# Performance work log

Hardware: AMD Instinct MI355X
Metric: run time of the kernel (lower is better)

The kernel has to match this reference:

```python
import jax, jax.numpy as jnp
import numpy as np

N_NODES = 50000
N_EDGES = 1600000
D_FEAT = 64
N_SCALARS = 4
N_GRAPHS = 64
HIDDEN = 128
OUT = 128


def setup_inputs() -> dict:
    key = jax.random.key(0)
    ks = jax.random.split(key, 8)
    x = jax.random.normal(ks[0], (N_NODES, D_FEAT), dtype=jnp.float32)
    scalars = jax.random.normal(ks[1], (N_GRAPHS, N_SCALARS), dtype=jnp.float32)
    batch = jnp.sort(jax.random.randint(ks[2], (N_NODES,), 0, N_GRAPHS))
    edge_index = jax.random.randint(ks[3], (2, N_EDGES), 0, N_NODES)
    d_in = 2 * (D_FEAT + N_SCALARS)  # 136: EdgeConv-style cat([x_i, x_j - x_i])
    W1 = jax.random.normal(ks[4], (d_in, HIDDEN), dtype=jnp.float32) * (1.0 / np.sqrt(d_in))
    b1 = jnp.zeros((HIDDEN,), dtype=jnp.float32)
    W2 = jax.random.normal(ks[5], (HIDDEN, OUT), dtype=jnp.float32) * (1.0 / np.sqrt(HIDDEN))
    b2 = jnp.zeros((OUT,), dtype=jnp.float32)
    return {"x": x, "scalars": scalars, "batch": batch, "edge_index": edge_index,
            "W1": W1, "b1": b1, "W2": W2, "b2": b2}


def reference(x, scalars, batch, edge_index, W1, b1, W2, b2):
    # _reshape_scalars: gather per-graph scalars to nodes via batch index
    s = scalars[batch]                       # [N, n_scalars]
    h = jnp.concatenate([x, s], axis=-1)     # [N, d_feat + n_scalars]
    src, dst = edge_index[0], edge_index[1]  # edge j -> i (PyG convention)
    h_i = h[dst]                             # target node features [E, F]
    h_j = h[src]                             # source node features [E, F]
    m_in = jnp.concatenate([h_i, h_j - h_i], axis=-1)  # [E, 2F]
    m = jax.nn.relu(m_in @ W1 + b1) @ W2 + b2          # edge MLP [E, OUT]
    out = jax.ops.segment_sum(m, dst, num_segments=x.shape[0])  # add-aggregation
    return out
```

## Files before the change

### kernel.cpp

```cpp
#include <hip/hip_runtime.h>

#define N_NODES   50000
#define N_EDGES   1600000
#define D_FEAT    64
#define N_SCALARS 4
#define HIDDEN    128
#define OUT_DIM   128
#define UV_DIM    256

#define SLICE_SH  6
#define SLICE_N   (1 << SLICE_SH)
#define NSLICE    ((N_NODES + SLICE_N - 1) >> SLICE_SH)
#define CAP       2560
#define CAPQ      1024
#define CHUNK     4096

#define N_WAVES   (N_NODES / 16)
#define G1_BLOCKS ((N_WAVES + 3) / 4)
#define BIN_BLOCKS ((N_EDGES + CHUNK - 1) / CHUNK)

typedef __attribute__((ext_vector_type(8))) _Float16 half8;
typedef __attribute__((ext_vector_type(2))) _Float16 half2v;
typedef __attribute__((ext_vector_type(4))) float    f32x4;

__device__ __forceinline__ float wf_elem(const float* W1, int k, int j) {
    float wb = W1[(k + 68) * HIDDEN + (j & 127)];
    return (j < HIDDEN) ? (W1[k * HIDDEN + j] - wb) : wb;
}

__device__ __forceinline__ unsigned char f2bf8(float f) {
    unsigned short h = __builtin_bit_cast(unsigned short, (_Float16)f);
    unsigned r = ((unsigned)h + 0x7Fu + ((h >> 8) & 1u)) >> 8;
    return (unsigned char)r;
}

__device__ __forceinline__ half2v bf8x2_to_h2(unsigned short w) {
    unsigned r = __builtin_amdgcn_perm(0u, (unsigned)w, 0x010C000Cu);
    return __builtin_bit_cast(half2v, r);
}

__global__ __launch_bounds__(256) void prep_kernel(
    const float* __restrict__ W1, const float* __restrict__ b1,
    const float* __restrict__ W2, const float* __restrict__ scalars,
    _Float16* __restrict__ WfT, _Float16* __restrict__ W2T,
    float* __restrict__ SG, int* __restrict__ tails)
{
    const int idx = blockIdx.x * 256 + threadIdx.x;
    {   int j = idx >> 6, k = idx & 63;
        WfT[idx] = (_Float16)wf_elem(W1, k, j); }
    {   int j = idx >> 7, k = idx & 127;
        W2T[idx] = (_Float16)W2[k * OUT_DIM + j]; }
    {   int g = idx >> 8, j = idx & 255;
        float s = (j < HIDDEN) ? b1[j] : 0.f;
        #pragma unroll
        for (int t = 0; t < N_SCALARS; ++t)
            s = fmaf(scalars[g * N_SCALARS + t], wf_elem(W1, D_FEAT + t, j), s);
        SG[idx] = s; }
    if (idx < NSLICE) tails[idx] = 0;
}

__global__ __launch_bounds__(256) void gemm1_bin(
    const float* __restrict__ x, const int* __restrict__ batch,
    const _Float16* __restrict__ WfT, const float* __restrict__ SG,
    _Float16* __restrict__ Uh, unsigned char* __restrict__ Vb8,
    const int* __restrict__ ei, int* __restrict__ tails,
    unsigned* __restrict__ glist)
{
    __shared__ unsigned buf[CHUNK];
    __shared__ int hist[NSLICE];
    __shared__ int binStart[NSLICE];
    __shared__ int cursor[NSLICE];
    __shared__ int gbase[NSLICE];
    __shared__ int scanTmp[256];

    const int tid = threadIdx.x;

    if (blockIdx.x < G1_BLOCKS) {
        const int wid = (blockIdx.x * 256 + tid) >> 6;
        if (wid >= N_WAVES) return;
        const int lane = tid & 63;
        const int quad = lane >> 4;
        const int l15  = lane & 15;
        const int row0 = wid * 16;

        f32x4 acc[16];
        #pragma unroll
        for (int c = 0; c < 16; ++c) { f32x4 z = {0.f,0.f,0.f,0.f}; acc[c] = z; }

        const float* xrow = x + (row0 + l15) * D_FEAT;
        #pragma unroll
        for (int t = 0; t < 2; ++t) {
            const int k0 = 32 * t + quad * 8;
            float4 a0 = *(const float4*)(xrow + k0);
            float4 a1 = *(const float4*)(xrow + k0 + 4);
            half8 af;
            af[0] = (_Float16)a0.x; af[1] = (_Float16)a0.y;
            af[2] = (_Float16)a0.z; af[3] = (_Float16)a0.w;
            af[4] = (_Float16)a1.x; af[5] = (_Float16)a1.y;
            af[6] = (_Float16)a1.z; af[7] = (_Float16)a1.w;
            #pragma unroll
            for (int c = 0; c < 16; ++c) {
                half8 bf = *(const half8*)(WfT + (c * 16 + l15) * 64 + k0);
                acc[c] = __builtin_amdgcn_mfma_f32_16x16x32_f16(af, bf, acc[c], 0, 0, 0);
            }
        }

        int bg[4];
        #pragma unroll
        for (int j = 0; j < 4; ++j) bg[j] = batch[row0 + quad * 4 + j];

        #pragma unroll
        for (int c = 0; c < 16; ++c) {
            const int col = c * 16 + l15;
            #pragma unroll
            for (int j = 0; j < 4; ++j) {
                const int n = row0 + quad * 4 + j;
                float v = acc[c][j] + SG[bg[j] * UV_DIM + col];
                if (col < HIDDEN) Uh[(n << 7) + col] = (_Float16)v;
                else              Vb8[(n << 7) + col - HIDDEN] = f2bf8(v);
            }
        }
        return;
    }

    const int e0  = (blockIdx.x - G1_BLOCKS) * CHUNK;
    const int nE  = min(CHUNK, N_EDGES - e0);

    for (int i = tid; i < NSLICE; i += 256) hist[i] = 0;
    __syncthreads();

    unsigned ent[CHUNK / 256];
    #pragma unroll
    for (int j = 0; j < CHUNK / 256; ++j) {
        int e = e0 + tid + j * 256;
        if (e < N_EDGES) {
            unsigned s = (unsigned)ei[e];
            unsigned d = (unsigned)ei[N_EDGES + e];
            ent[j] = (d << 16) | s;
            atomicAdd(&hist[d >> SLICE_SH], 1);
        } else {
            ent[j] = 0xFFFFFFFFu;
        }
    }
    __syncthreads();

    const int base4 = tid * 4;
    int loc[4];
    int sum = 0;
    #pragma unroll
    for (int k = 0; k < 4; ++k) {
        int b = base4 + k;
        loc[k] = (b < NSLICE) ? hist[b] : 0;
        sum += loc[k];
    }
    scanTmp[tid] = sum;
    __syncthreads();
    for (int d = 1; d < 256; d <<= 1) {
        int v = (tid >= d) ? scanTmp[tid - d] : 0;
        __syncthreads();
        scanTmp[tid] += v;
        __syncthreads();
    }
    int run = (tid == 0) ? 0 : scanTmp[tid - 1];
    #pragma unroll
    for (int k = 0; k < 4; ++k) {
        int b = base4 + k;
        if (b < NSLICE) { binStart[b] = run; cursor[b] = run; run += loc[k]; }
    }
    __syncthreads();

    #pragma unroll
    for (int j = 0; j < CHUNK / 256; ++j) {
        if (ent[j] != 0xFFFFFFFFu) {
            int sl = (int)(ent[j] >> (16 + SLICE_SH));
            int pos = atomicAdd(&cursor[sl], 1);
            buf[pos] = ent[j];
        }
    }
    __syncthreads();

    for (int s = tid; s < NSLICE; s += 256) {
        int c = hist[s];
        if (c > 0) gbase[s] = atomicAdd(&tails[s], c);
    }
    __syncthreads();

    for (int i = tid; i < nE; i += 256) {
        unsigned e = buf[i];
        int sl = (int)(e >> (16 + SLICE_SH));
        int di = gbase[sl] + (i - binStart[sl]);
        if (di < CAP) glist[(size_t)sl * CAP + di] = e;
    }
}

__global__ __launch_bounds__(256) void agg_gemm2(
    const unsigned* __restrict__ glist, const int* __restrict__ tails,
    const _Float16* __restrict__ Uh, const unsigned char* __restrict__ Vb8,
    const _Float16* __restrict__ W2T, const float* __restrict__ b2,
    float* __restrict__ out)
{
    __shared__ int h16[16];
    __shared__ int start16[16];
    __shared__ int cur16[16];
    __shared__ unsigned sbuf[CAPQ];
    __shared__ _Float16 aggA[16][136];

    const int slice = blockIdx.x;
    const int yq    = blockIdx.y;
    const int node0 = (slice << SLICE_SH) + yq * 16;
    const int tid   = threadIdx.x;
    const unsigned* lst = glist + (size_t)slice * CAP;
    const int cnt = min(tails[slice], CAP);

    if (tid < 16) h16[tid] = 0;
    __syncthreads();
    for (int i = tid; i < cnt; i += 256) {
        unsigned e = lst[i];
        int dl = (e >> 16) & 63;
        if ((dl >> 4) == yq) atomicAdd(&h16[dl & 15], 1);
    }
    __syncthreads();
    if (tid == 0) {
        int run = 0;
        #pragma unroll
        for (int b = 0; b < 16; ++b) {
            run = (run + 3) & ~3;
            start16[b] = run; cur16[b] = run;
            run += h16[b];
        }
    }
    __syncthreads();
    for (int i = tid; i < cnt; i += 256) {
        unsigned e = lst[i];
        int dl = (e >> 16) & 63;
        if ((dl >> 4) == yq) {
            int pos = atomicAdd(&cur16[dl & 15], 1);
            if (pos < CAPQ) sbuf[pos] = e & 0xFFFFu;
        }
    }
    __syncthreads();

    const int wave = tid >> 6;
    const int lane = tid & 63;
    const int quad = lane >> 4;
    const int l15  = lane & 15;
    const int c2   = lane * 2;
    const half2v zero = {(_Float16)0, (_Float16)0};
    const unsigned char* Vc = Vb8 + c2;

    #pragma unroll
    for (int i = 0; i < 4; ++i) {
        const int b = wave * 4 + i;
        const int n = node0 + b;
        half2v u2 = zero, acc2 = zero;
        int gb = start16[b];
        int gc = h16[b];
        if (n < N_NODES) u2 = *(const half2v*)(Uh + (n << 7) + c2);
        else gc = 0;
        int p = gb, pe = min(gb + gc, CAPQ);
        for (; p + 8 <= pe; p += 8) {
            uint4 q0 = *(const uint4*)&sbuf[p];
            uint4 q1 = *(const uint4*)&sbuf[p + 4];
            unsigned short w0 = *(const unsigned short*)(Vc + (q0.x << 7));
            unsigned short w1 = *(const unsigned short*)(Vc + (q0.y << 7));
            unsigned short w2 = *(const unsigned short*)(Vc + (q0.z << 7));
            unsigned short w3 = *(const unsigned short*)(Vc + (q0.w << 7));
            unsigned short w4 = *(const unsigned short*)(Vc + (q1.x << 7));
            unsigned short w5 = *(const unsigned short*)(Vc + (q1.y << 7));
            unsigned short w6 = *(const unsigned short*)(Vc + (q1.z << 7));
            unsigned short w7 = *(const unsigned short*)(Vc + (q1.w << 7));
            half2v m0 = __builtin_elementwise_max(u2 + bf8x2_to_h2(w0), zero);
            half2v m1 = __builtin_elementwise_max(u2 + bf8x2_to_h2(w1), zero);
            half2v m2 = __builtin_elementwise_max(u2 + bf8x2_to_h2(w2), zero);
            half2v m3 = __builtin_elementwise_max(u2 + bf8x2_to_h2(w3), zero);
            half2v m4 = __builtin_elementwise_max(u2 + bf8x2_to_h2(w4), zero);
            half2v m5 = __builtin_elementwise_max(u2 + bf8x2_to_h2(w5), zero);
            half2v m6 = __builtin_elementwise_max(u2 + bf8x2_to_h2(w6), zero);
            half2v m7 = __builtin_elementwise_max(u2 + bf8x2_to_h2(w7), zero);
            acc2 += ((m0 + m1) + (m2 + m3)) + ((m4 + m5) + (m6 + m7));
        }
        for (; p + 4 <= pe; p += 4) {
            uint4 q0 = *(const uint4*)&sbuf[p];
            unsigned short w0 = *(const unsigned short*)(Vc + (q0.x << 7));
            unsigned short w1 = *(const unsigned short*)(Vc + (q0.y << 7));
            unsigned short w2 = *(const unsigned short*)(Vc + (q0.z << 7));
            unsigned short w3 = *(const unsigned short*)(Vc + (q0.w << 7));
            acc2 += (__builtin_elementwise_max(u2 + bf8x2_to_h2(w0), zero)
                   + __builtin_elementwise_max(u2 + bf8x2_to_h2(w1), zero))
                  + (__builtin_elementwise_max(u2 + bf8x2_to_h2(w2), zero)
                   + __builtin_elementwise_max(u2 + bf8x2_to_h2(w3), zero));
        }
        for (; p < pe; ++p) {
            unsigned s0 = sbuf[p];
            unsigned short w0 = *(const unsigned short*)(Vc + (s0 << 7));
            acc2 += __builtin_elementwise_max(u2 + bf8x2_to_h2(w0), zero);
        }
        *(half2v*)&aggA[b][c2] = acc2;
    }
    __syncthreads();

    f32x4 accm[2];
    {   f32x4 z = {0.f,0.f,0.f,0.f}; accm[0] = z; accm[1] = z; }
    #pragma unroll
    for (int t = 0; t < 4; ++t) {
        const int k0 = 32 * t + quad * 8;
        half8 af = *(const half8*)&aggA[l15][k0];
        #pragma unroll
        for (int c = 0; c < 2; ++c) {
            const int ct = wave * 2 + c;
            half8 bf = *(const half8*)(W2T + ((ct * 16 + l15) << 7) + k0);
            accm[c] = __builtin_amdgcn_mfma_f32_16x16x32_f16(af, bf, accm[c], 0, 0, 0);
        }
    }
    int dgj[4];
    #pragma unroll
    for (int j = 0; j < 4; ++j) dgj[j] = h16[quad * 4 + j];

    #pragma unroll
    for (int c = 0; c < 2; ++c) {
        const int col = (wave * 2 + c) * 16 + l15;
        const float bb = b2[col];
        #pragma unroll
        for (int j = 0; j < 4; ++j) {
            const int n = node0 + quad * 4 + j;
            if (n < N_NODES)
                out[(size_t)n * OUT_DIM + col] = accm[c][j] + bb * (float)dgj[j];
        }
    }
}

extern "C" void kernel_launch(void* const* d_in, const int* in_sizes, int n_in,
                              void* d_out, int out_size, void* d_ws, size_t ws_size,
                              hipStream_t stream)
{
    const float* x       = (const float*)d_in[0];
    const float* scalars = (const float*)d_in[1];
    const int*   batch   = (const int*)d_in[2];
    const int*   ei      = (const int*)d_in[3];
    const float* W1      = (const float*)d_in[4];
    const float* b1      = (const float*)d_in[5];
    const float* W2      = (const float*)d_in[6];
    const float* b2      = (const float*)d_in[7];
    float*       out     = (float*)d_out;

    _Float16*      Uh    = (_Float16*)d_ws;
    unsigned char* Vb8   = (unsigned char*)(Uh + (size_t)N_NODES * HIDDEN);
    unsigned*      glist = (unsigned*)(Vb8 + (size_t)N_NODES * HIDDEN);
    _Float16*      WfT   = (_Float16*)(glist + (size_t)NSLICE * CAP);
    _Float16*      W2T   = WfT + 256 * 64;
    float*         SG    = (float*)(W2T + 128 * 128);
    int*           tails = (int*)(SG + 64 * UV_DIM);

    prep_kernel<<<64, 256, 0, stream>>>(W1, b1, W2, scalars, WfT, W2T, SG, tails);

    gemm1_bin<<<G1_BLOCKS + BIN_BLOCKS, 256, 0, stream>>>(
        x, batch, WfT, SG, Uh, Vb8, ei, tails, glist);

    agg_gemm2<<<dim3(NSLICE, 4), 256, 0, stream>>>(
        glist, tails, Uh, Vb8, W2T, b2, out);
}
```

Before: 180.6 us.

## Bucket edges into fixed per-node shared lists with 512-thread half-slice blocks

The aggregation kernel now covers 32 nodes per block with 512 threads instead of 16 nodes with 256 threads, which halves how many times each slice's edge list is read from global memory. The histogram, prefix-scan and second scatter pass are replaced by a single pass that appends 16-bit source indices into fixed-capacity per-node shared lists (CAPL=80). The gather loop reads packed ushort indices, and the GEMM2 work is split across 8 waves as 2 row groups by 4 column groups. The risk is that edges beyond 80 per node are silently dropped, which is safe only if in-degree stays under that cap (mean degree here is 32).

```diff
diff --git a/kernel.cpp b/kernel.cpp
--- a/kernel.cpp
+++ b/kernel.cpp
@@ -12,7 +12,7 @@
 #define SLICE_N   (1 << SLICE_SH)
 #define NSLICE    ((N_NODES + SLICE_N - 1) >> SLICE_SH)
 #define CAP       2560
-#define CAPQ      1024
+#define CAPL      80
 #define CHUNK     4096
 
 #define N_WAVES   (N_NODES / 16)
@@ -193,49 +193,32 @@
     }
 }
 
-__global__ __launch_bounds__(256) void agg_gemm2(
+__global__ __launch_bounds__(512) void agg_gemm2(
     const unsigned* __restrict__ glist, const int* __restrict__ tails,
     const _Float16* __restrict__ Uh, const unsigned char* __restrict__ Vb8,
     const _Float16* __restrict__ W2T, const float* __restrict__ b2,
     float* __restrict__ out)
 {
-    __shared__ int h16[16];
-    __shared__ int start16[16];
-    __shared__ int cur16[16];
-    __shared__ unsigned sbuf[CAPQ];
-    __shared__ _Float16 aggA[16][136];
+    __shared__ unsigned short lists[32 * CAPL];
+    __shared__ _Float16 aggA[32][136];
+    __shared__ int cur32[32];
 
     const int slice = blockIdx.x;
-    const int yq    = blockIdx.y;
-    const int node0 = (slice << SLICE_SH) + yq * 16;
+    const int half  = blockIdx.y;
+    const int node0 = (slice << SLICE_SH) + half * 32;
     const int tid   = threadIdx.x;
     const unsigned* lst = glist + (size_t)slice * CAP;
     const int cnt = min(tails[slice], CAP);
 
-    if (tid < 16) h16[tid] = 0;
-    __syncthreads();
-    for (int i = tid; i < cnt; i += 256) {
+    if (tid < 32) cur32[tid] = 0;
+    __syncthreads();
+
+    for (int i = tid; i < cnt; i += 512) {
         unsigned e = lst[i];
-        int dl = (e >> 16) & 63;
-        if ((dl >> 4) == yq) atomicAdd(&h16[dl & 15], 1);
-    }
-    __syncthreads();
-    if (tid == 0) {
-        int run = 0;
-        #pragma unroll
-        for (int b = 0; b < 16; ++b) {
-            run = (run + 3) & ~3;
-            start16[b] = run; cur16[b] = run;
-            run += h16[b];
-        }
-    }
-    __syncthreads();
-    for (int i = tid; i < cnt; i += 256) {
-        unsigned e = lst[i];
-        int dl = (e >> 16) & 63;
-        if ((dl >> 4) == yq) {
-            int pos = atomicAdd(&cur16[dl & 15], 1);
-            if (pos < CAPQ) sbuf[pos] = e & 0xFFFFu;
+        if (((e >> 21) & 1u) == (unsigned)half) {
+            int b = (e >> 16) & 31;
+            int pos = atomicAdd(&cur32[b], 1);
+            if (pos < CAPL) lists[b * CAPL + pos] = (unsigned short)(e & 0xFFFFu);
         }
     }
     __syncthreads();
@@ -252,23 +235,21 @@
     for (int i = 0; i < 4; ++i) {
         const int b = wave * 4 + i;
         const int n = node0 + b;
+        const int gc = (n < N_NODES) ? min(cur32[b], CAPL) : 0;
         half2v u2 = zero, acc2 = zero;
-        int gb = start16[b];
-        int gc = h16[b];
         if (n < N_NODES) u2 = *(const half2v*)(Uh + (n << 7) + c2);
-        else gc = 0;
-        int p = gb, pe = min(gb + gc, CAPQ);
+        int p = b * CAPL;
+        const int pe = p + gc;
         for (; p + 8 <= pe; p += 8) {
-            uint4 q0 = *(const uint4*)&sbuf[p];
-            uint4 q1 = *(const uint4*)&sbuf[p + 4];
-            unsigned short w0 = *(const unsigned short*)(Vc + (q0.x << 7));
-            unsigned short w1 = *(const unsigned short*)(Vc + (q0.y << 7));
-            unsigned short w2 = *(const unsigned short*)(Vc + (q0.z << 7));
-            unsigned short w3 = *(const unsigned short*)(Vc + (q0.w << 7));
-            unsigned short w4 = *(const unsigned short*)(Vc + (q1.x << 7));
-            unsigned short w5 = *(const unsigned short*)(Vc + (q1.y << 7));
-            unsigned short w6 = *(const unsigned short*)(Vc + (q1.z << 7));
-            unsigned short w7 = *(const unsigned short*)(Vc + (q1.w << 7));
+            uint4 q = *(const uint4*)&lists[p];
+            unsigned short w0 = *(const unsigned short*)(Vc + ((q.x & 0xFFFFu) << 7));
+            unsigned short w1 = *(const unsigned short*)(Vc + ((q.x >> 16)     << 7));
+            unsigned short w2 = *(const unsigned short*)(Vc + ((q.y & 0xFFFFu) << 7));
+            unsigned short w3 = *(const unsigned short*)(Vc + ((q.y >> 16)     << 7));
+            unsigned short w4 = *(const unsigned short*)(Vc + ((q.z & 0xFFFFu) << 7));
+            unsigned short w5 = *(const unsigned short*)(Vc + ((q.z >> 16)     << 7));
+            unsigned short w6 = *(const unsigned short*)(Vc + ((q.w & 0xFFFFu) << 7));
+            unsigned short w7 = *(const unsigned short*)(Vc + ((q.w >> 16)     << 7));
             half2v m0 = __builtin_elementwise_max(u2 + bf8x2_to_h2(w0), zero);
             half2v m1 = __builtin_elementwise_max(u2 + bf8x2_to_h2(w1), zero);
             half2v m2 = __builtin_elementwise_max(u2 + bf8x2_to_h2(w2), zero);
@@ -280,18 +261,18 @@
             acc2 += ((m0 + m1) + (m2 + m3)) + ((m4 + m5) + (m6 + m7));
         }
         for (; p + 4 <= pe; p += 4) {
-            uint4 q0 = *(const uint4*)&sbuf[p];
-            unsigned short w0 = *(const unsigned short*)(Vc + (q0.x << 7));
-            unsigned short w1 = *(const unsigned short*)(Vc + (q0.y << 7));
-            unsigned short w2 = *(const unsigned short*)(Vc + (q0.z << 7));
-            unsigned short w3 = *(const unsigned short*)(Vc + (q0.w << 7));
+            uint2 q = *(const uint2*)&lists[p];
+            unsigned short w0 = *(const unsigned short*)(Vc + ((q.x & 0xFFFFu) << 7));
+            unsigned short w1 = *(const unsigned short*)(Vc + ((q.x >> 16)     << 7));
+            unsigned short w2 = *(const unsigned short*)(Vc + ((q.y & 0xFFFFu) << 7));
+            unsigned short w3 = *(const unsigned short*)(Vc + ((q.y >> 16)     << 7));
             acc2 += (__builtin_elementwise_max(u2 + bf8x2_to_h2(w0), zero)
                    + __builtin_elementwise_max(u2 + bf8x2_to_h2(w1), zero))
                   + (__builtin_elementwise_max(u2 + bf8x2_to_h2(w2), zero)
                    + __builtin_elementwise_max(u2 + bf8x2_to_h2(w3), zero));
         }
         for (; p < pe; ++p) {
-            unsigned s0 = sbuf[p];
+            unsigned s0 = (unsigned)lists[p];
             unsigned short w0 = *(const unsigned short*)(Vc + (s0 << 7));
             acc2 += __builtin_elementwise_max(u2 + bf8x2_to_h2(w0), zero);
         }
@@ -299,30 +280,35 @@
     }
     __syncthreads();
 
+    const int rg = wave >> 2;
+    const int cg = wave & 3;
     f32x4 accm[2];
     {   f32x4 z = {0.f,0.f,0.f,0.f}; accm[0] = z; accm[1] = z; }
     #pragma unroll
     for (int t = 0; t < 4; ++t) {
         const int k0 = 32 * t + quad * 8;
-        half8 af = *(const half8*)&aggA[l15][k0];
+        half8 af = *(const half8*)&aggA[rg * 16 + l15][k0];
         #pragma unroll
         for (int c = 0; c < 2; ++c) {
-            const int ct = wave * 2 + c;
+            const int ct = cg * 2 + c;
             half8 bf = *(const half8*)(W2T + ((ct * 16 + l15) << 7) + k0);
             accm[c] = __builtin_amdgcn_mfma_f32_16x16x32_f16(af, bf, accm[c], 0, 0, 0);
         }
     }
     int dgj[4];
     #pragma unroll
-    for (int j = 0; j < 4; ++j) dgj[j] = h16[quad * 4 + j];
+    for (int j = 0; j < 4; ++j) {
+        int b = rg * 16 + quad * 4 + j;
+        dgj[j] = min(cur32[b], CAPL);
+    }
 
     #pragma unroll
     for (int c = 0; c < 2; ++c) {
-        const int col = (wave * 2 + c) * 16 + l15;
+        const int col = (cg * 2 + c) * 16 + l15;
         const float bb = b2[col];
         #pragma unroll
         for (int j = 0; j < 4; ++j) {
-            const int n = node0 + quad * 4 + j;
+            const int n = node0 + rg * 16 + quad * 4 + j;
             if (n < N_NODES)
                 out[(size_t)n * OUT_DIM + col] = accm[c][j] + bb * (float)dgj[j];
         }
@@ -356,6 +342,6 @@
     gemm1_bin<<<G1_BLOCKS + BIN_BLOCKS, 256, 0, stream>>>(
         x, batch, WfT, SG, Uh, Vb8, ei, tails, glist);
 
-    agg_gemm2<<<dim3(NSLICE, 4), 256, 0, stream>>>(
+    agg_gemm2<<<dim3(NSLICE, 2), 512, 0, stream>>>(
         glist, tails, Uh, Vb8, W2T, b2, out);
 }
```

After: 185.7 us. 2.8% more time.

## Add per-node rebinning kernel and simplify aggregation to read per-node neighbor lists

Applied to the files above, without the earlier changes.

A new rebin kernel runs once per 64-node slice. It sorts the slice's edge list into fixed-capacity per-node lists of 16-bit source ids, written in place over the old list, plus a degree array. The aggregation kernel then runs one block per 16 nodes and reads each node's list directly. This removes the four-fold rescanning, shared-memory histograms and atomics that each quarter-slice block used to do, at the cost of one extra kernel launch. Separately, the GEMM1 epilogue takes a fast path when all 16 rows belong to the same graph, loading the scalar row once instead of one lookup per row.

```diff
diff --git a/kernel.cpp b/kernel.cpp
--- a/kernel.cpp
+++ b/kernel.cpp
@@ -12,12 +12,14 @@
 #define SLICE_N   (1 << SLICE_SH)
 #define NSLICE    ((N_NODES + SLICE_N - 1) >> SLICE_SH)
 #define CAP       2560
-#define CAPQ      1024
+#define CAPN      80
+#define CAPN_DW   (CAPN / 2)
 #define CHUNK     4096
 
 #define N_WAVES   (N_NODES / 16)
 #define G1_BLOCKS ((N_WAVES + 3) / 4)
 #define BIN_BLOCKS ((N_EDGES + CHUNK - 1) / CHUNK)
+#define AGG_BLOCKS (N_NODES / 16)
 
 typedef __attribute__((ext_vector_type(8))) _Float16 half8;
 typedef __attribute__((ext_vector_type(2))) _Float16 half2v;
@@ -105,19 +107,37 @@
             }
         }
 
-        int bg[4];
-        #pragma unroll
-        for (int j = 0; j < 4; ++j) bg[j] = batch[row0 + quad * 4 + j];
-
-        #pragma unroll
-        for (int c = 0; c < 16; ++c) {
-            const int col = c * 16 + l15;
+        const int gA = batch[row0];
+        const int gB = batch[row0 + 15];
+
+        if (gA == gB) {
+            const float* SGr = SG + gA * UV_DIM;
             #pragma unroll
-            for (int j = 0; j < 4; ++j) {
-                const int n = row0 + quad * 4 + j;
-                float v = acc[c][j] + SG[bg[j] * UV_DIM + col];
-                if (col < HIDDEN) Uh[(n << 7) + col] = (_Float16)v;
-                else              Vb8[(n << 7) + col - HIDDEN] = f2bf8(v);
+            for (int c = 0; c < 16; ++c) {
+                const int col = c * 16 + l15;
+                const float sg = SGr[col];
+                #pragma unroll
+                for (int j = 0; j < 4; ++j) {
+                    const int n = row0 + quad * 4 + j;
+                    float v = acc[c][j] + sg;
+                    if (col < HIDDEN) Uh[(n << 7) + col] = (_Float16)v;
+                    else              Vb8[(n << 7) + col - HIDDEN] = f2bf8(v);
+                }
+            }
+        } else {
+            int bg[4];
+            #pragma unroll
+            for (int j = 0; j < 4; ++j) bg[j] = batch[row0 + quad * 4 + j];
+            #pragma unroll
+            for (int c = 0; c < 16; ++c) {
+                const int col = c * 16 + l15;
+                #pragma unroll
+                for (int j = 0; j < 4; ++j) {
+                    const int n = row0 + quad * 4 + j;
+                    float v = acc[c][j] + SG[bg[j] * UV_DIM + col];
+                    if (col < HIDDEN) Uh[(n << 7) + col] = (_Float16)v;
+                    else              Vb8[(n << 7) + col - HIDDEN] = f2bf8(v);
+                }
             }
         }
         return;
@@ -193,110 +213,117 @@
     }
 }
 
+__global__ __launch_bounds__(256) void rebin_kernel(
+    const unsigned* glist, const int* __restrict__ tails,
+    unsigned short* nlist, int* __restrict__ degN)
+{
+    __shared__ unsigned short lists[64 * CAPN];
+    __shared__ int cur[64];
+
+    const int sl  = blockIdx.x;
+    const int tid = threadIdx.x;
+    const unsigned* lst = glist + (size_t)sl * CAP;
+    const int cnt = min(tails[sl], CAP);
+
+    if (tid < 64) cur[tid] = 0;
+    __syncthreads();
+
+    for (int i = tid; i < cnt; i += 256) {
+        unsigned e = lst[i];
+        int b = (e >> 16) & 63;
+        int pos = atomicAdd(&cur[b], 1);
+        if (pos < CAPN) lists[b * CAPN + pos] = (unsigned short)e;
+    }
+    __syncthreads();
+
+    unsigned* N32 = (unsigned*)nlist + (size_t)sl * (64 * CAPN_DW);
+    const unsigned* L32 = (const unsigned*)lists;
+    #pragma unroll
+    for (int k = 0; k < (64 * CAPN_DW) / 256; ++k)
+        N32[tid + k * 256] = L32[tid + k * 256];
+
+    if (tid < 64) degN[sl * 64 + tid] = min(cur[tid], CAPN);
+}
+
 __global__ __launch_bounds__(256) void agg_gemm2(
-    const unsigned* __restrict__ glist, const int* __restrict__ tails,
+    const unsigned short* __restrict__ nlist, const int* __restrict__ degN,
     const _Float16* __restrict__ Uh, const unsigned char* __restrict__ Vb8,
     const _Float16* __restrict__ W2T, const float* __restrict__ b2,
     float* __restrict__ out)
 {
-    __shared__ int h16[16];
-    __shared__ int start16[16];
-    __shared__ int cur16[16];
-    __shared__ unsigned sbuf[CAPQ];
     __shared__ _Float16 aggA[16][136];
-
-    const int slice = blockIdx.x;
-    const int yq    = blockIdx.y;
-    const int node0 = (slice << SLICE_SH) + yq * 16;
+    __shared__ int deg16[16];
+
+    const int node0 = blockIdx.x << 4;
     const int tid   = threadIdx.x;
-    const unsigned* lst = glist + (size_t)slice * CAP;
-    const int cnt = min(tails[slice], CAP);
-
-    if (tid < 16) h16[tid] = 0;
-    __syncthreads();
-    for (int i = tid; i < cnt; i += 256) {
-        unsigned e = lst[i];
-        int dl = (e >> 16) & 63;
-        if ((dl >> 4) == yq) atomicAdd(&h16[dl & 15], 1);
-    }
-    __syncthreads();
-    if (tid == 0) {
-        int run = 0;
-        #pragma unroll
-        for (int b = 0; b < 16; ++b) {
-            run = (run + 3) & ~3;
-            start16[b] = run; cur16[b] = run;
-            run += h16[b];
-        }
-    }
-    __syncthreads();
-    for (int i = tid; i < cnt; i += 256) {
-        unsigned e = lst[i];
-        int dl = (e >> 16) & 63;
-        if ((dl >> 4) == yq) {
-            int pos = atomicAdd(&cur16[dl & 15], 1);
-            if (pos < CAPQ) sbuf[pos] = e & 0xFFFFu;
-        }
-    }
-    __syncthreads();
-
-    const int wave = tid >> 6;
-    const int lane = tid & 63;
-    const int quad = lane >> 4;
-    const int l15  = lane & 15;
-    const int c2   = lane * 2;
+    const int wave  = tid >> 6;
+    const int lane  = tid & 63;
+    const int quad  = lane >> 4;
+    const int l15   = lane & 15;
+    const int c2    = lane * 2;
     const half2v zero = {(_Float16)0, (_Float16)0};
-    const unsigned char* Vc = Vb8 + c2;
+
+    if (tid < 16) deg16[tid] = min(degN[node0 + tid], CAPN);
+
+#define VLOAD(s) (*(const unsigned short*)(Vb8 + ((size_t)(s) << 7) + c2))
 
     #pragma unroll
     for (int i = 0; i < 4; ++i) {
-        const int b = wave * 4 + i;
-        const int n = node0 + b;
-        half2v u2 = zero, acc2 = zero;
-        int gb = start16[b];
-        int gc = h16[b];
-        if (n < N_NODES) u2 = *(const half2v*)(Uh + (n << 7) + c2);
-        else gc = 0;
-        int p = gb, pe = min(gb + gc, CAPQ);
-        for (; p + 8 <= pe; p += 8) {
-            uint4 q0 = *(const uint4*)&sbuf[p];
-            uint4 q1 = *(const uint4*)&sbuf[p + 4];
-            unsigned short w0 = *(const unsigned short*)(Vc + (q0.x << 7));
-            unsigned short w1 = *(const unsigned short*)(Vc + (q0.y << 7));
-            unsigned short w2 = *(const unsigned short*)(Vc + (q0.z << 7));
-            unsigned short w3 = *(const unsigned short*)(Vc + (q0.w << 7));
-            unsigned short w4 = *(const unsigned short*)(Vc + (q1.x << 7));
-            unsigned short w5 = *(const unsigned short*)(Vc + (q1.y << 7));
-            unsigned short w6 = *(const unsigned short*)(Vc + (q1.z << 7));
-            unsigned short w7 = *(const unsigned short*)(Vc + (q1.w << 7));
-            half2v m0 = __builtin_elementwise_max(u2 + bf8x2_to_h2(w0), zero);
-            half2v m1 = __builtin_elementwise_max(u2 + bf8x2_to_h2(w1), zero);
-            half2v m2 = __builtin_elementwise_max(u2 + bf8x2_to_h2(w2), zero);
-            half2v m3 = __builtin_elementwise_max(u2 + bf8x2_to_h2(w3), zero);
-            half2v m4 = __builtin_elementwise_max(u2 + bf8x2_to_h2(w4), zero);
-            half2v m5 = __builtin_elementwise_max(u2 + bf8x2_to_h2(w5), zero);
-            half2v m6 = __builtin_elementwise_max(u2 + bf8x2_to_h2(w6), zero);
-            half2v m7 = __builtin_elementwise_max(u2 + bf8x2_to_h2(w7), zero);
-            acc2 += ((m0 + m1) + (m2 + m3)) + ((m4 + m5) + (m6 + m7));
-        }
-        for (; p + 4 <= pe; p += 4) {
-            uint4 q0 = *(const uint4*)&sbuf[p];
-            unsigned short w0 = *(const unsigned short*)(Vc + (q0.x << 7));
-            unsigned short w1 = *(const unsigned short*)(Vc + (q0.y << 7));
-            unsigned short w2 = *(const unsigned short*)(Vc + (q0.z << 7));
-            unsigned short w3 = *(const unsigned short*)(Vc + (q0.w << 7));
-            acc2 += (__builtin_elementwise_max(u2 + bf8x2_to_h2(w0), zero)
-                   + __builtin_elementwise_max(u2 + bf8x2_to_h2(w1), zero))
-                  + (__builtin_elementwise_max(u2 + bf8x2_to_h2(w2), zero)
-                   + __builtin_elementwise_max(u2 + bf8x2_to_h2(w3), zero));
-        }
-        for (; p < pe; ++p) {
-            unsigned s0 = sbuf[p];
-            unsigned short w0 = *(const unsigned short*)(Vc + (s0 << 7));
-            acc2 += __builtin_elementwise_max(u2 + bf8x2_to_h2(w0), zero);
+        const int b  = wave * 4 + i;
+        const int nu = __builtin_amdgcn_readfirstlane(node0 + b);
+        const int deg = min(degN[nu], CAPN);
+        const unsigned* Lw = (const unsigned*)nlist + (size_t)nu * CAPN_DW;
+        half2v u2 = *(const half2v*)(Uh + ((size_t)nu << 7) + c2);
+        half2v acc2 = zero;
+
+        const int nf = deg >> 4;
+        for (int ch = 0; ch < nf; ++ch) {
+            const unsigned* Lc = Lw + ch * 8;
+            unsigned d0 = Lc[0], d1 = Lc[1], d2 = Lc[2], d3 = Lc[3];
+            unsigned d4 = Lc[4], d5 = Lc[5], d6 = Lc[6], d7 = Lc[7];
+            unsigned short w0  = VLOAD(d0 & 0xFFFFu), w1  = VLOAD(d0 >> 16);
+            unsigned short w2  = VLOAD(d1 & 0xFFFFu), w3  = VLOAD(d1 >> 16);
+            unsigned short w4  = VLOAD(d2 & 0xFFFFu), w5  = VLOAD(d2 >> 16);
+            unsigned short w6  = VLOAD(d3 & 0xFFFFu), w7  = VLOAD(d3 >> 16);
+            unsigned short w8  = VLOAD(d4 & 0xFFFFu), w9  = VLOAD(d4 >> 16);
+            unsigned short w10 = VLOAD(d5 & 0xFFFFu), w11 = VLOAD(d5 >> 16);
+            unsigned short w12 = VLOAD(d6 & 0xFFFFu), w13 = VLOAD(d6 >> 16);
+            unsigned short w14 = VLOAD(d7 & 0xFFFFu), w15 = VLOAD(d7 >> 16);
+            half2v m0  = __builtin_elementwise_max(u2 + bf8x2_to_h2(w0),  zero);
+            half2v m1  = __builtin_elementwise_max(u2 + bf8x2_to_h2(w1),  zero);
+            half2v m2  = __builtin_elementwise_max(u2 + bf8x2_to_h2(w2),  zero);
+            half2v m3  = __builtin_elementwise_max(u2 + bf8x2_to_h2(w3),  zero);
+            half2v m4  = __builtin_elementwise_max(u2 + bf8x2_to_h2(w4),  zero);
+            half2v m5  = __builtin_elementwise_max(u2 + bf8x2_to_h2(w5),  zero);
+            half2v m6  = __builtin_elementwise_max(u2 + bf8x2_to_h2(w6),  zero);
+            half2v m7  = __builtin_elementwise_max(u2 + bf8x2_to_h2(w7),  zero);
+            half2v m8  = __builtin_elementwise_max(u2 + bf8x2_to_h2(w8),  zero);
+            half2v m9  = __builtin_elementwise_max(u2 + bf8x2_to_h2(w9),  zero);
+            half2v m10 = __builtin_elementwise_max(u2 + bf8x2_to_h2(w10), zero);
+            half2v m11 = __builtin_elementwise_max(u2 + bf8x2_to_h2(w11), zero);
+            half2v m12 = __builtin_elementwise_max(u2 + bf8x2_to_h2(w12), zero);
+            half2v m13 = __builtin_elementwise_max(u2 + bf8x2_to_h2(w13), zero);
+            half2v m14 = __builtin_elementwise_max(u2 + bf8x2_to_h2(w14), zero);
+            half2v m15 = __builtin_elementwise_max(u2 + bf8x2_to_h2(w15), zero);
+            half2v s0 = (m0 + m1) + (m2 + m3);
+            half2v s1 = (m4 + m5) + (m6 + m7);
+            half2v s2 = (m8 + m9) + (m10 + m11);
+            half2v s3 = (m12 + m13) + (m14 + m15);
+            acc2 += (s0 + s1) + (s2 + s3);
+        }
+        const int rem = deg & 15;
+        if (rem) {
+            const unsigned* Lc = Lw + nf * 8;
+            for (int e = 0; e < rem; ++e) {
+                unsigned dw = Lc[e >> 1];
+                unsigned s = (e & 1) ? (dw >> 16) : (dw & 0xFFFFu);
+                unsigned short w = VLOAD(s);
+                acc2 += __builtin_elementwise_max(u2 + bf8x2_to_h2(w), zero);
+            }
         }
         *(half2v*)&aggA[b][c2] = acc2;
     }
+#undef VLOAD
     __syncthreads();
 
     f32x4 accm[2];
@@ -314,7 +341,7 @@
     }
     int dgj[4];
     #pragma unroll
-    for (int j = 0; j < 4; ++j) dgj[j] = h16[quad * 4 + j];
+    for (int j = 0; j < 4; ++j) dgj[j] = deg16[quad * 4 + j];
 
     #pragma unroll
     for (int c = 0; c < 2; ++c) {
@@ -323,8 +350,7 @@
         #pragma unroll
         for (int j = 0; j < 4; ++j) {
             const int n = node0 + quad * 4 + j;
-            if (n < N_NODES)
-                out[(size_t)n * OUT_DIM + col] = accm[c][j] + bb * (float)dgj[j];
+            out[(size_t)n * OUT_DIM + col] = accm[c][j] + bb * (float)dgj[j];
         }
     }
 }
@@ -343,19 +369,23 @@
     const float* b2      = (const float*)d_in[7];
     float*       out     = (float*)d_out;
 
-    _Float16*      Uh    = (_Float16*)d_ws;
-    unsigned char* Vb8   = (unsigned char*)(Uh + (size_t)N_NODES * HIDDEN);
-    unsigned*      glist = (unsigned*)(Vb8 + (size_t)N_NODES * HIDDEN);
-    _Float16*      WfT   = (_Float16*)(glist + (size_t)NSLICE * CAP);
-    _Float16*      W2T   = WfT + 256 * 64;
-    float*         SG    = (float*)(W2T + 128 * 128);
-    int*           tails = (int*)(SG + 64 * UV_DIM);
+    _Float16*       Uh    = (_Float16*)d_ws;
+    unsigned char*  Vb8   = (unsigned char*)(Uh + (size_t)N_NODES * HIDDEN);
+    unsigned*       glist = (unsigned*)(Vb8 + (size_t)N_NODES * HIDDEN);
+    unsigned short* nlist = (unsigned short*)glist;
+    int*            degN  = (int*)(glist + (size_t)NSLICE * CAP);
+    _Float16*       WfT   = (_Float16*)(degN + NSLICE * SLICE_N);
+    _Float16*       W2T   = WfT + 256 * 64;
+    float*          SG    = (float*)(W2T + 128 * 128);
+    int*            tails = (int*)(SG + 64 * UV_DIM);
 
     prep_kernel<<<64, 256, 0, stream>>>(W1, b1, W2, scalars, WfT, W2T, SG, tails);
 
     gemm1_bin<<<G1_BLOCKS + BIN_BLOCKS, 256, 0, stream>>>(
         x, batch, WfT, SG, Uh, Vb8, ei, tails, glist);
 
-    agg_gemm2<<<dim3(NSLICE, 4), 256, 0, stream>>>(
-        glist, tails, Uh, Vb8, W2T, b2, out);
-}
+    rebin_kernel<<<NSLICE, 256, 0, stream>>>(glist, tails, nlist, degN);
+
+    agg_gemm2<<<AGG_BLOCKS, 256, 0, stream>>>(
+        nlist, degN, Uh, Vb8, W2T, b2, out);
+}
```

Measured after the change: 180.3 us. About the same (-0.2%).
